# Kernel optimization log

Hardware: AMD Instinct MI355X
Metric: run time of the kernel (lower is better)

The kernel has to match this reference:

```python
import jax, jax.numpy as jnp
import numpy as np

B, N, L, E, U, G, R, D, C = 64, 50000, 8, 100000, 20000, 20000, 64, 16, 2


def setup_inputs() -> dict:
    rng = np.random.default_rng(0)
    key = jax.random.key(0)
    ks = jax.random.split(key, 10)
    # index structures (duplicate-free where the torch code assumes uniqueness)
    gene_map = jnp.asarray(rng.choice(N, G, replace=False).astype(np.int32))
    dst_unique = jnp.stack([jnp.asarray(rng.choice(N, U, replace=False).astype(np.int32)) for _ in range(L)])
    root_ids = jnp.asarray(rng.choice(N, R, replace=False).astype(np.int32))
    src = jax.random.randint(ks[0], (L, E), 0, N, dtype=jnp.int32)
    dst_pos = jax.random.randint(ks[1], (L, E), 0, U, dtype=jnp.int32)
    # data and parameters
    X_gene_batch = jax.random.normal(ks[2], (B, G), jnp.float32)
    w_in = jax.random.normal(ks[3], (D,), jnp.float32) * 0.5   # Linear(1, d) weight
    b_in = jax.random.normal(ks[4], (D,), jnp.float32) * 0.1
    W = jax.random.normal(ks[5], (L, D, D), jnp.float32) * (1.0 / np.sqrt(D))  # xavier-ish
    bias = jnp.zeros((N, D), jnp.float32)
    W_head = jax.random.normal(ks[6], (C, R * D), jnp.float32) * (1.0 / np.sqrt(R * D))
    b_head = jnp.zeros((C,), jnp.float32)
    return {
        "X_gene_batch": X_gene_batch, "w_in": w_in, "b_in": b_in, "W": W,
        "bias": bias, "W_head": W_head, "b_head": b_head,
        "gene_map": gene_map, "src": src, "dst_pos": dst_pos,
        "dst_unique": dst_unique, "root_ids": root_ids,
    }


def reference(X_gene_batch, w_in, b_in, W, bias, W_head, b_head,
              gene_map, src, dst_pos, dst_unique, root_ids):
    Bn = X_gene_batch.shape[0]
    n_nodes, d = bias.shape
    n_layers = W.shape[0]
    u = dst_unique.shape[1]
    # _init_state_vector: h=0, scatter in_proj(X[...,None]) at gene_map
    gene_emb = X_gene_batch[..., None] * w_in + b_in          # [B, G, d]
    h = jnp.zeros((Bn, n_nodes, d), X_gene_batch.dtype)
    h = h.at[:, gene_map].set(gene_emb)
    for li in range(n_layers):
        h_src = h[:, src[li]]                                  # gather [B, E, d]
        msg = jnp.einsum('bed,df->bef', h_src, W[li])          # small dxd matmul
        agg = jnp.zeros((Bn, u, d), h.dtype).at[:, dst_pos[li]].add(msg)  # scatter-add
        h_dst = jnp.tanh(agg + bias[dst_unique[li]][None])     # bias lookup + tanh (dropout=0)
        h = h.at[:, dst_unique[li]].set(h_dst)                 # write back
    feat = h[:, root_ids].reshape(Bn, -1)                      # roots_concat readout
    return feat @ W_head.T + b_head                            # [B, C]
```

## Files before the change

### kernel.cpp

```cpp
#include <hip/hip_runtime.h>
#include <hip/hip_fp16.h>
#include <cmath>

constexpr int B_ = 64, N_ = 50000, L_ = 8, E_ = 100000, U_ = 20000, G_ = 20000, R_ = 64, D_ = 16, C_ = 2;
constexpr int EPL_ = E_ + 3 * U_ + 4096;
constexpr int EPLG_ = EPL_ / 4 + 64;
constexpr int GPW = 8;
constexpr int GCAP = EPL_ / 4;
constexpr int SW = (GCAP + GPW - 1) / GPW;

constexpr int BC = 64;
constexpr int F = BC * 2;

constexpr int HBC = 32;
constexpr int FH = HBC * 2;
constexpr int DST0 = 1 + G_;
constexpr int AROWS = DST0 + L_ * U_;

__device__ __forceinline__ float tanh_fast(float x) {
  float e = __expf(2.0f * x);
  return 1.0f - 2.0f * __builtin_amdgcn_rcpf(e + 1.0f);
}


__global__ __launch_bounds__(256) void hist_kernel(
    const int* __restrict__ dst_pos, int* __restrict__ cnt,
    int* __restrict__ rank) {
  int e = blockIdx.x * 256 + threadIdx.x;
  int li = blockIdx.y;
  if (e >= E_) return;
  rank[li * E_ + e] = atomicAdd(&cnt[li * U_ + dst_pos[li * E_ + e]], 1);
}

__global__ __launch_bounds__(1024) void scan_kernel(
    const int* __restrict__ cnt, int* __restrict__ offs) {
  __shared__ int sums[1024];
  int li = blockIdx.x, t = threadIdx.x;
  int base = t * 20;
  int v[20];
  int s = 0;
#pragma unroll
  for (int i = 0; i < 20; ++i) {
    int idx = base + i;
    int c = (idx < U_) ? cnt[li * U_ + idx] : -1;
    int pc = (c < 0) ? 0 : ((c == 0) ? 4 : ((c + 3) & ~3));
    v[i] = s;
    s += pc;
  }
  sums[t] = s;
  __syncthreads();
  for (int off = 1; off < 1024; off <<= 1) {
    int o = (t >= off) ? sums[t - off] : 0;
    __syncthreads();
    sums[t] += o;
    __syncthreads();
  }
  int excl = sums[t] - s;
#pragma unroll
  for (int i = 0; i < 20; ++i) {
    int idx = base + i;
    if (idx < U_) offs[li * (U_ + 1) + idx] = excl + v[i];
  }
  if (t == 1023) offs[li * (U_ + 1) + U_] = sums[1023];
}

__global__ __launch_bounds__(256) void scatter_kernel(
    const int* __restrict__ dst_pos, const int* __restrict__ src,
    const int* __restrict__ offs, const int* __restrict__ rank,
    int* __restrict__ ssrc) {
  int e = blockIdx.x * 256 + threadIdx.x;
  int li = blockIdx.y;
  if (e >= E_) return;
  int u = dst_pos[li * E_ + e];
  int p = offs[li * (U_ + 1) + u] + rank[li * E_ + e];
  ssrc[(size_t)li * EPL_ + p] = src[li * E_ + e];
}

__global__ __launch_bounds__(256) void pad_fill_ug_k(
    const int* __restrict__ cnt, const int* __restrict__ offs,
    int* __restrict__ ssrc, int* __restrict__ ug) {
  int t = blockIdx.x * 256 + threadIdx.x;
  if (t < L_ * U_) {
    int li = t / U_, u = t % U_;
    int start = offs[li * (U_ + 1) + u];
    int end = start + cnt[li * U_ + u];
    int pend = offs[li * (U_ + 1) + u + 1];
    int* sp = ssrc + (size_t)li * EPL_;
    for (int p = end; p < pend; ++p) sp[p] = N_;
    int* ugp = ug + (size_t)li * EPLG_;
    for (int g = start >> 2; g < (pend >> 2); ++g) ugp[g] = u;
  } else {
    int t2 = t - L_ * U_;
    int li = t2 >> 8, j = t2 & 255;
    if (li < L_) {
      int* sp = ssrc + (size_t)li * EPL_;
      int ptot = offs[li * (U_ + 1) + U_];
      int pos = ptot + j;
      if (pos < EPL_) sp[pos] = N_;
      sp[EPL_ - 256 + j] = N_;
    }
  }
}


__global__ __launch_bounds__(256) void mark_k(
    const int* __restrict__ dst_unique, const int* __restrict__ gene_map,
    int* __restrict__ wmask, int* __restrict__ posarr, int* __restrict__ lw0) {
  int t = blockIdx.x * 256 + threadIdx.x;
  if (t < L_ * U_) {
    int li = t / U_, u = t % U_;
    int n = dst_unique[t];
    posarr[li * N_ + n] = u;
    atomicOr(&wmask[n], 1 << li);
  } else {
    int g = t - L_ * U_;
    if (g < G_) lw0[gene_map[g]] = 1 + g;
  }
}

__global__ __launch_bounds__(256) void remap_k(
    const int* __restrict__ offs, const int* __restrict__ wmask,
    const int* __restrict__ posarr, const int* __restrict__ lw0,
    int* __restrict__ ssrc) {
  int p = blockIdx.x * 256 + threadIdx.x;
  int li = blockIdx.y;
  if (p >= EPL_) return;
  int ptot = offs[li * (U_ + 1) + U_];
  if (p >= ptot + 256 && p < EPL_ - 256) return;
  int* sp = ssrc + (size_t)li * EPL_;
  int s = sp[p];
  int m = wmask[s] & ((1 << li) - 1);
  int phys;
  if (m) {
    int lj = 31 - __clz(m);
    phys = DST0 + lj * U_ + posarr[lj * N_ + s];
  } else {
    phys = lw0[s];
  }
  sp[p] = phys;
}

#define PHASE(VACC, VLD, IDLD, IDPF, NUCUR)          \
  {                                                  \
    loadRows(VLD, IDLD);                             \
    IDPF = *(const int4*)(sp + 4 * CLG(g + 4));      \
    int nuCur = NUCUR;                               \
    NUCUR = ugp[CLG(g + 3) + 1];                     \
    accum(VACC);                                     \
    if (nuCur != curU) {                             \
      flushu(curU);                                  \
      if (g + 1 >= gstop) return;                    \
      curU = nuCur;                                  \
    }                                                \
    ++g;                                             \
  }


__global__ __launch_bounds__(256) void gene_a(
    const float* __restrict__ X, const float* __restrict__ w_in,
    const float* __restrict__ b_in, float4* __restrict__ h4, int half) {
  int t = blockIdx.x * 256 + threadIdx.x;
  if (t >= G_ * HBC) return;
  int b = t % HBC;
  int g = t / HBC;
  float x = X[(half * HBC + b) * G_ + g];
  float4 out[2];
  __half2* oh = reinterpret_cast<__half2*>(out);
#pragma unroll
  for (int k = 0; k < 8; ++k) {
    float r0 = fmaf(x, w_in[2 * k], b_in[2 * k]);
    float r1 = fmaf(x, w_in[2 * k + 1], b_in[2 * k + 1]);
    oh[k] = __float22half2_rn(make_float2(r0, r1));
  }
  h4[(size_t)(1 + g) * FH + b * 2] = out[0];
  h4[(size_t)(1 + g) * FH + b * 2 + 1] = out[1];
}

__global__ __launch_bounds__(256, 2) void gfused_a(
    const float4* __restrict__ h4, const int* __restrict__ ug,
    const int* __restrict__ ssrc, const float* __restrict__ W,
    const float* __restrict__ bias, const int* __restrict__ dst_unique,
    float4* __restrict__ o4, int li) {
  __shared__ float Wlds[256];
  int tid = threadIdx.x;
  Wlds[tid] = W[li * 256 + tid];
  __syncthreads();
  int lane = tid & 63;
  int dh = lane & 1;
  int wv = __builtin_amdgcn_readfirstlane(blockIdx.x * 4 + (tid >> 6));
  const int* ugp = ug + (size_t)li * EPLG_;
  const int* sp = ssrc + (size_t)li * EPL_;
  const int* du = dst_unique + (size_t)li * U_;

  int g0 = wv * GPW, gend = g0 + GPW;
  int prevU = (g0 == 0) ? -2 : ugp[g0 - 1];
  int g = g0;
  while (g < gend && ugp[g] == prevU) ++g;
  if (g >= gend) return;
  int curU = ugp[g];
  if (curU < 0) return;
  int uend = ugp[gend - 1];
  int gstop;
  if (uend < 0) {
    gstop = g;
    while (ugp[gstop] >= 0) ++gstop;
  } else {
    gstop = gend;
    while (ugp[gstop] == uend) ++gstop;
  }

  __half2 acc[2][4];
  const __half2 z = __half2half2(__float2half(0.f));
#pragma unroll
  for (int j = 0; j < 2; ++j)
#pragma unroll
    for (int k = 0; k < 4; ++k) acc[j][k] = z;

  auto flushu = [&](int u) {
    int node = du[u];
    float biasv[8];
    {
      const float4* bp = (const float4*)(bias + (size_t)node * 16 + dh * 8);
      float4 q0 = bp[0], q1 = bp[1];
      biasv[0] = q0.x; biasv[1] = q0.y; biasv[2] = q0.z; biasv[3] = q0.w;
      biasv[4] = q1.x; biasv[5] = q1.y; biasv[6] = q1.z; biasv[7] = q1.w;
    }
    float a8[8];
#pragma unroll
    for (int k = 0; k < 4; ++k) {
      float2 f0 = __half22float2(acc[0][k]);
      float2 f1 = __half22float2(acc[1][k]);
      __half2 hv = __float22half2_rn(make_float2(f0.x + f1.x, f0.y + f1.y));
      float2 fa = __half22float2(hv);
      a8[2 * k] = fa.x; a8[2 * k + 1] = fa.y;
    }
    float pm[16];
#pragma unroll
    for (int j = 0; j < 16; ++j) pm[j] = 0.f;
#pragma unroll
    for (int dd = 0; dd < 8; ++dd) {
      float s = a8[dd];
      const float4* wr = (const float4*)&Wlds[(dh * 8 + dd) * 16];
      float4 w0 = wr[0], w1 = wr[1], w2 = wr[2], w3 = wr[3];
      pm[0] = fmaf(s, w0.x, pm[0]);  pm[1] = fmaf(s, w0.y, pm[1]);
      pm[2] = fmaf(s, w0.z, pm[2]);  pm[3] = fmaf(s, w0.w, pm[3]);
      pm[4] = fmaf(s, w1.x, pm[4]);  pm[5] = fmaf(s, w1.y, pm[5]);
      pm[6] = fmaf(s, w1.z, pm[6]);  pm[7] = fmaf(s, w1.w, pm[7]);
      pm[8] = fmaf(s, w2.x, pm[8]);  pm[9] = fmaf(s, w2.y, pm[9]);
      pm[10] = fmaf(s, w2.z, pm[10]); pm[11] = fmaf(s, w2.w, pm[11]);
      pm[12] = fmaf(s, w3.x, pm[12]); pm[13] = fmaf(s, w3.y, pm[13]);
      pm[14] = fmaf(s, w3.z, pm[14]); pm[15] = fmaf(s, w3.w, pm[15]);
    }
    float m8[8];
#pragma unroll
    for (int jj = 0; jj < 8; ++jj) {
      float s0 = pm[jj] + __shfl_xor(pm[jj], 1, 64);
      float s1 = pm[8 + jj] + __shfl_xor(pm[8 + jj], 1, 64);
      m8[jj] = dh ? s1 : s0;
    }
    float4 outv;
    __half2* ov = reinterpret_cast<__half2*>(&outv);
#pragma unroll
    for (int k = 0; k < 4; ++k) {
      ov[k] = __float22half2_rn(
          make_float2(tanh_fast(m8[2 * k] + biasv[2 * k]),
                      tanh_fast(m8[2 * k + 1] + biasv[2 * k + 1])));
    }
    o4[(size_t)(DST0 + li * U_ + u) * FH + lane] = outv;
#pragma unroll
    for (int j = 0; j < 2; ++j)
#pragma unroll
      for (int k = 0; k < 4; ++k) acc[j][k] = z;
  };

  auto loadRows = [&](float4 (&v)[4], int4 id) {
    v[0] = h4[(size_t)id.x * FH + lane];
    v[1] = h4[(size_t)id.y * FH + lane];
    v[2] = h4[(size_t)id.z * FH + lane];
    v[3] = h4[(size_t)id.w * FH + lane];
  };
  auto accum = [&](const float4 (&v)[4]) {
#pragma unroll
    for (int j = 0; j < 4; ++j) {
      const __half2* p = reinterpret_cast<const __half2*>(&v[j]);
#pragma unroll
      for (int k = 0; k < 4; ++k)
        acc[j & 1][k] = __hadd2(acc[j & 1][k], p[k]);
    }
  };
  auto CLG = [&](int q) { return (q < GCAP) ? q : GCAP - 1; };

  int4 id0 = *(const int4*)(sp + 4 * g);
  int4 id1 = *(const int4*)(sp + 4 * CLG(g + 1));
  int4 idP = *(const int4*)(sp + 4 * CLG(g + 2));
  int4 idQ = *(const int4*)(sp + 4 * CLG(g + 3));
  int4 idR;
  int nuA = ugp[g + 1];
  int nuB = ugp[CLG(g + 1) + 1];
  int nuC = ugp[CLG(g + 2) + 1];

  float4 va[4], vb[4], vc[4];
  loadRows(va, id0);
  loadRows(vb, id1);

  for (;;) {
    PHASE(va, vc, idP, idR, nuA)
    PHASE(vb, va, idQ, idP, nuB)
    PHASE(vc, vb, idR, idQ, nuC)
  }
}

__global__ __launch_bounds__(64) void head_a(
    const float4* __restrict__ h4, const float* __restrict__ W_head,
    const float* __restrict__ b_head, const int* __restrict__ root_ids,
    const int* __restrict__ wmask, const int* __restrict__ posarr,
    const int* __restrict__ lw0, int half, float* __restrict__ out) {
  int bl = blockIdx.x;
  int r = threadIdx.x;
  int node = root_ids[r];
  int m = wmask[node];
  int phys;
  if (m) {
    int lj = 31 - __clz(m);
    phys = DST0 + lj * U_ + posarr[lj * N_ + node];
  } else {
    phys = lw0[node];
  }
  float4 p0 = h4[(size_t)phys * FH + bl * 2];
  float4 p1 = h4[(size_t)phys * FH + bl * 2 + 1];
  float v[16];
  const __half2* ph0 = reinterpret_cast<const __half2*>(&p0);
  const __half2* ph1 = reinterpret_cast<const __half2*>(&p1);
#pragma unroll
  for (int k = 0; k < 4; ++k) {
    float2 f0 = __half22float2(ph0[k]);
    float2 f1 = __half22float2(ph1[k]);
    v[2 * k] = f0.x; v[2 * k + 1] = f0.y;
    v[8 + 2 * k] = f1.x; v[8 + 2 * k + 1] = f1.y;
  }
  float acc0 = 0.f, acc1 = 0.f;
#pragma unroll
  for (int d = 0; d < 16; ++d) {
    acc0 = fmaf(v[d], W_head[r * 16 + d], acc0);
    acc1 = fmaf(v[d], W_head[1024 + r * 16 + d], acc1);
  }
  for (int off = 32; off; off >>= 1) {
    acc0 += __shfl_down(acc0, off, 64);
    acc1 += __shfl_down(acc1, off, 64);
  }
  if (r == 0) {
    int gb = half * HBC + bl;
    out[gb * 2 + 0] = acc0 + b_head[0];
    out[gb * 2 + 1] = acc1 + b_head[1];
  }
}


__global__ __launch_bounds__(256) void gene_c(
    const float* __restrict__ X, const float* __restrict__ w_in,
    const float* __restrict__ b_in, const int* __restrict__ gene_map,
    float4* __restrict__ h4) {
  int t = blockIdx.x * 256 + threadIdx.x;
  if (t >= G_ * BC) return;
  int b = t % BC;
  int g = t / BC;
  float x = X[b * G_ + g];
  int node = gene_map[g];
  float4 out[2];
  __half2* oh = reinterpret_cast<__half2*>(out);
#pragma unroll
  for (int k = 0; k < 8; ++k) {
    float r0 = fmaf(x, w_in[2 * k], b_in[2 * k]);
    float r1 = fmaf(x, w_in[2 * k + 1], b_in[2 * k + 1]);
    oh[k] = __float22half2_rn(make_float2(r0, r1));
  }
  h4[(size_t)node * F + b * 2] = out[0];
  h4[(size_t)node * F + b * 2 + 1] = out[1];
}

__global__ __launch_bounds__(256, 2) void gather_c(
    const float4* __restrict__ h4, const int* __restrict__ ug,
    const int* __restrict__ ssrc, float4* __restrict__ agg4, int li) {
  int tid = threadIdx.x;
  int lane = tid & 63;
  int wv = __builtin_amdgcn_readfirstlane(blockIdx.x * 4 + (tid >> 6));
  const int* ugp = ug + (size_t)li * EPLG_;
  const int* sp = ssrc + (size_t)li * EPL_;

  int g0 = wv * GPW, gend = g0 + GPW;
  int prevU = (g0 == 0) ? -2 : ugp[g0 - 1];
  int g = g0;
  while (g < gend && ugp[g] == prevU) ++g;
  if (g >= gend) return;
  int curU = ugp[g];
  if (curU < 0) return;
  int uend = ugp[gend - 1];
  int gstop;
  if (uend < 0) {
    gstop = g;
    while (ugp[gstop] >= 0) ++gstop;
  } else {
    gstop = gend;
    while (ugp[gstop] == uend) ++gstop;
  }

  __half2 acc[2][2][4];
  const __half2 z = __half2half2(__float2half(0.f));
#pragma unroll
  for (int j = 0; j < 2; ++j)
#pragma unroll
    for (int r = 0; r < 2; ++r)
#pragma unroll
      for (int k = 0; k < 4; ++k) acc[j][r][k] = z;

  auto flushu = [&](int u) {
#pragma unroll
    for (int r = 0; r < 2; ++r) {
      float4 outv;
      __half2* ov = reinterpret_cast<__half2*>(&outv);
#pragma unroll
      for (int k = 0; k < 4; ++k) {
        float2 f0 = __half22float2(acc[0][r][k]);
        float2 f1 = __half22float2(acc[1][r][k]);
        ov[k] = __float22half2_rn(make_float2(f0.x + f1.x, f0.y + f1.y));
      }
      agg4[(size_t)u * F + lane + r * 64] = outv;
    }
#pragma unroll
    for (int j = 0; j < 2; ++j)
#pragma unroll
      for (int r = 0; r < 2; ++r)
#pragma unroll
        for (int k = 0; k < 4; ++k) acc[j][r][k] = z;
  };
  auto loadRows = [&](float4 (&v)[4][2], int4 id) {
    v[0][0] = h4[(size_t)id.x * F + lane]; v[0][1] = h4[(size_t)id.x * F + lane + 64];
    v[1][0] = h4[(size_t)id.y * F + lane]; v[1][1] = h4[(size_t)id.y * F + lane + 64];
    v[2][0] = h4[(size_t)id.z * F + lane]; v[2][1] = h4[(size_t)id.z * F + lane + 64];
    v[3][0] = h4[(size_t)id.w * F + lane]; v[3][1] = h4[(size_t)id.w * F + lane + 64];
  };
  auto accum = [&](const float4 (&v)[4][2]) {
#pragma unroll
    for (int j = 0; j < 4; ++j)
#pragma unroll
      for (int r = 0; r < 2; ++r) {
        const __half2* p = reinterpret_cast<const __half2*>(&v[j][r]);
#pragma unroll
        for (int k = 0; k < 4; ++k)
          acc[j & 1][r][k] = __hadd2(acc[j & 1][r][k], p[k]);
      }
  };
  auto CLG = [&](int q) { return (q < GCAP) ? q : GCAP - 1; };

  int4 id0 = *(const int4*)(sp + 4 * g);
  int4 id1 = *(const int4*)(sp + 4 * CLG(g + 1));
  int4 idP = *(const int4*)(sp + 4 * CLG(g + 2));
  int4 idQ = *(const int4*)(sp + 4 * CLG(g + 3));
  int4 idR;
  int nuA = ugp[g + 1];
  int nuB = ugp[CLG(g + 1) + 1];
  int nuC = ugp[CLG(g + 2) + 1];

  float4 va[4][2], vb[4][2], vc[4][2];
  loadRows(va, id0);
  loadRows(vb, id1);

  for (;;) {
    PHASE(va, vc, idP, idR, nuA)
    PHASE(vb, va, idQ, idP, nuB)
    PHASE(vc, vb, idR, idQ, nuC)
  }
}
#undef PHASE

__global__ __launch_bounds__(256) void dense_c(
    const float4* __restrict__ agg4, const float* __restrict__ W,
    const float* __restrict__ bias, const int* __restrict__ dst_unique,
    float4* __restrict__ h4, int li) {
  __shared__ float Wlds[256];
  int tid = threadIdx.x;
  Wlds[tid] = W[li * 256 + tid];
  __syncthreads();
  int u = __builtin_amdgcn_readfirstlane(blockIdx.x * 4 + (tid >> 6));
  int b = tid & 63;
  float4 c0 = agg4[(size_t)u * F + b * 2];
  float4 c1 = agg4[(size_t)u * F + b * 2 + 1];
  float a[16];
  {
    const __half2* p0 = reinterpret_cast<const __half2*>(&c0);
    const __half2* p1 = reinterpret_cast<const __half2*>(&c1);
#pragma unroll
    for (int k = 0; k < 4; ++k) {
      float2 f0 = __half22float2(p0[k]);
      float2 f1 = __half22float2(p1[k]);
      a[2 * k] = f0.x; a[2 * k + 1] = f0.y;
      a[8 + 2 * k] = f1.x; a[8 + 2 * k + 1] = f1.y;
    }
  }
  float m[16];
#pragma unroll
  for (int j = 0; j < 16; ++j) m[j] = 0.f;
#pragma unroll
  for (int d = 0; d < 16; ++d) {
    float s = a[d];
    const float4* wr = (const float4*)&Wlds[d * 16];
    float4 w0 = wr[0], w1 = wr[1], w2 = wr[2], w3 = wr[3];
    m[0] = fmaf(s, w0.x, m[0]);  m[1] = fmaf(s, w0.y, m[1]);
    m[2] = fmaf(s, w0.z, m[2]);  m[3] = fmaf(s, w0.w, m[3]);
    m[4] = fmaf(s, w1.x, m[4]);  m[5] = fmaf(s, w1.y, m[5]);
    m[6] = fmaf(s, w1.z, m[6]);  m[7] = fmaf(s, w1.w, m[7]);
    m[8] = fmaf(s, w2.x, m[8]);  m[9] = fmaf(s, w2.y, m[9]);
    m[10] = fmaf(s, w2.z, m[10]); m[11] = fmaf(s, w2.w, m[11]);
    m[12] = fmaf(s, w3.x, m[12]); m[13] = fmaf(s, w3.y, m[13]);
    m[14] = fmaf(s, w3.z, m[14]); m[15] = fmaf(s, w3.w, m[15]);
  }
  int node = dst_unique[li * U_ + u];
  const float4* bp = (const float4*)(bias + (size_t)node * 16);
  float4 b0 = bp[0], b1 = bp[1], b2 = bp[2], b3 = bp[3];
  float bb[16] = {b0.x, b0.y, b0.z, b0.w, b1.x, b1.y, b1.z, b1.w,
                  b2.x, b2.y, b2.z, b2.w, b3.x, b3.y, b3.z, b3.w};
  float4 o0, o1;
  __half2* ov0 = reinterpret_cast<__half2*>(&o0);
  __half2* ov1 = reinterpret_cast<__half2*>(&o1);
#pragma unroll
  for (int k = 0; k < 4; ++k) {
    ov0[k] = __float22half2_rn(make_float2(tanh_fast(m[2 * k] + bb[2 * k]),
                                           tanh_fast(m[2 * k + 1] + bb[2 * k + 1])));
    ov1[k] = __float22half2_rn(make_float2(tanh_fast(m[8 + 2 * k] + bb[8 + 2 * k]),
                                           tanh_fast(m[8 + 2 * k + 1] + bb[8 + 2 * k + 1])));
  }
  h4[(size_t)node * F + b * 2] = o0;
  h4[(size_t)node * F + b * 2 + 1] = o1;
}

__global__ __launch_bounds__(64) void head_c(
    const float4* __restrict__ h4, const float* __restrict__ W_head,
    const float* __restrict__ b_head, const int* __restrict__ root_ids,
    float* __restrict__ out) {
  int bl = blockIdx.x;
  int r = threadIdx.x;
  int node = root_ids[r];
  float4 p0 = h4[(size_t)node * F + bl * 2];
  float4 p1 = h4[(size_t)node * F + bl * 2 + 1];
  float v[16];
  const __half2* ph0 = reinterpret_cast<const __half2*>(&p0);
  const __half2* ph1 = reinterpret_cast<const __half2*>(&p1);
#pragma unroll
  for (int k = 0; k < 4; ++k) {
    float2 f0 = __half22float2(ph0[k]);
    float2 f1 = __half22float2(ph1[k]);
    v[2 * k] = f0.x; v[2 * k + 1] = f0.y;
    v[8 + 2 * k] = f1.x; v[8 + 2 * k + 1] = f1.y;
  }
  float acc0 = 0.f, acc1 = 0.f;
#pragma unroll
  for (int d = 0; d < 16; ++d) {
    acc0 = fmaf(v[d], W_head[r * 16 + d], acc0);
    acc1 = fmaf(v[d], W_head[1024 + r * 16 + d], acc1);
  }
  for (int off = 32; off; off >>= 1) {
    acc0 += __shfl_down(acc0, off, 64);
    acc1 += __shfl_down(acc1, off, 64);
  }
  if (r == 0) {
    out[bl * 2 + 0] = acc0 + b_head[0];
    out[bl * 2 + 1] = acc1 + b_head[1];
  }
}

__global__ void zero_out_k(float* out, int n) {
  int t = blockIdx.x * 256 + threadIdx.x;
  if (t < n) out[t] = 0.f;
}


static size_t csr_aux_bytes() {
  return (size_t)L_ * U_ * 4 +
         (size_t)L_ * (U_ + 1) * 4 +
         (size_t)L_ * E_ * 4 +
         (size_t)L_ * EPL_ * 4 +
         (size_t)L_ * EPLG_ * 4;
}
static size_t arena_bytes() {
  return (size_t)AROWS * FH * 16 + csr_aux_bytes() +
         (size_t)2 * (N_ + 1) * 4 +
         (size_t)L_ * N_ * 4;
}
static size_t classic_bytes() {
  return (size_t)(N_ + 1) * F * 16 + (size_t)U_ * F * 16 + csr_aux_bytes();
}

extern "C" void kernel_launch(void* const* d_in, const int* in_sizes, int n_in,
                              void* d_out, int out_size, void* d_ws, size_t ws_size,
                              hipStream_t stream) {
  const float* X = (const float*)d_in[0];
  const float* w_in = (const float*)d_in[1];
  const float* b_in = (const float*)d_in[2];
  const float* W = (const float*)d_in[3];
  const float* bias = (const float*)d_in[4];
  const float* W_head = (const float*)d_in[5];
  const float* b_head = (const float*)d_in[6];
  const int* gene_map = (const int*)d_in[7];
  const int* src = (const int*)d_in[8];
  const int* dst_pos = (const int*)d_in[9];
  const int* dst_unique = (const int*)d_in[10];
  const int* root_ids = (const int*)d_in[11];
  float* out = (float*)d_out;

  dim3 egrid((E_ + 255) / 256, L_);
  const int pf_grid = (L_ * U_ + L_ * 256 + 255) / 256;
  const int gather_grid = (SW + 3) / 4;

  if (ws_size >= arena_bytes()) {
    char* ws = (char*)d_ws;
    float4* arena = (float4*)ws;
    size_t off = (size_t)AROWS * FH * 16;
    int* cnt = (int*)(ws + off);    off += (size_t)L_ * U_ * 4;
    int* offs = (int*)(ws + off);   off += (size_t)L_ * (U_ + 1) * 4;
    int* rank = (int*)(ws + off);   off += (size_t)L_ * E_ * 4;
    int* ssrc = (int*)(ws + off);   off += (size_t)L_ * EPL_ * 4;
    int* ug = (int*)(ws + off);     off += (size_t)L_ * EPLG_ * 4;
    int* wmask = (int*)(ws + off);  off += (size_t)(N_ + 1) * 4;
    int* lw0 = (int*)(ws + off);    off += (size_t)(N_ + 1) * 4;
    int* posarr = (int*)(ws + off);

    hipMemsetAsync(cnt, 0, (size_t)L_ * U_ * 4, stream);
    hipMemsetAsync(ug, 0xFF, (size_t)L_ * EPLG_ * 4, stream);
    hipMemsetAsync(wmask, 0, (size_t)2 * (N_ + 1) * 4, stream);
    hipMemsetAsync(arena, 0, (size_t)FH * 16, stream);

    hist_kernel<<<egrid, 256, 0, stream>>>(dst_pos, cnt, rank);
    scan_kernel<<<L_, 1024, 0, stream>>>(cnt, offs);
    scatter_kernel<<<egrid, 256, 0, stream>>>(dst_pos, src, offs, rank, ssrc);
    pad_fill_ug_k<<<pf_grid, 256, 0, stream>>>(cnt, offs, ssrc, ug);
    mark_k<<<(L_ * U_ + G_ + 255) / 256, 256, 0, stream>>>(dst_unique, gene_map,
                                                           wmask, posarr, lw0);
    dim3 rgrid((EPL_ + 255) / 256, L_);
    remap_k<<<rgrid, 256, 0, stream>>>(offs, wmask, posarr, lw0, ssrc);

    for (int half = 0; half < 2; ++half) {
      gene_a<<<(G_ * HBC + 255) / 256, 256, 0, stream>>>(X, w_in, b_in, arena,
                                                         half);
      for (int li = 0; li < L_; ++li) {
        gfused_a<<<gather_grid, 256, 0, stream>>>(arena, ug, ssrc, W, bias,
                                                  dst_unique, arena, li);
      }
      head_a<<<HBC, 64, 0, stream>>>(arena, W_head, b_head, root_ids, wmask,
                                     posarr, lw0, half, out);
    }
  } else if (ws_size >= classic_bytes()) {
    const size_t h_bytes = (size_t)(N_ + 1) * F * 16;
    const size_t agg_bytes = (size_t)U_ * F * 16;
    char* ws = (char*)d_ws;
    float4* h4 = (float4*)ws;
    float4* agg4 = (float4*)(ws + h_bytes);
    size_t off = h_bytes + agg_bytes;
    int* cnt = (int*)(ws + off);  off += (size_t)L_ * U_ * 4;
    int* offs = (int*)(ws + off); off += (size_t)L_ * (U_ + 1) * 4;
    int* rank = (int*)(ws + off); off += (size_t)L_ * E_ * 4;
    int* ssrc = (int*)(ws + off); off += (size_t)L_ * EPL_ * 4;
    int* ug = (int*)(ws + off);

    hipMemsetAsync(cnt, 0, (size_t)L_ * U_ * 4, stream);
    hipMemsetAsync(ug, 0xFF, (size_t)L_ * EPLG_ * 4, stream);
    hipMemsetAsync(h4, 0, h_bytes, stream);
    hist_kernel<<<egrid, 256, 0, stream>>>(dst_pos, cnt, rank);
    scan_kernel<<<L_, 1024, 0, stream>>>(cnt, offs);
    scatter_kernel<<<egrid, 256, 0, stream>>>(dst_pos, src, offs, rank, ssrc);
    pad_fill_ug_k<<<pf_grid, 256, 0, stream>>>(cnt, offs, ssrc, ug);
    gene_c<<<(G_ * BC + 255) / 256, 256, 0, stream>>>(X, w_in, b_in, gene_map, h4);
    const int dense_grid = U_ * BC / 256;
    for (int li = 0; li < L_; ++li) {
      gather_c<<<gather_grid, 256, 0, stream>>>(h4, ug, ssrc, agg4, li);
      dense_c<<<dense_grid, 256, 0, stream>>>(agg4, W, bias, dst_unique, h4, li);
    }
    head_c<<<BC, 64, 0, stream>>>(h4, W_head, b_head, root_ids, out);
  } else {
    zero_out_k<<<(out_size + 255) / 256, 256, 0, stream>>>(out, out_size);
  }
}
```

Before: 550.7 us.

## Fuse CSR preprocessing kernels and coalesce gene embedding input reads

Merges histogram and node-marking into one launch. Replaces the stored per-edge rank with an atomic cursor on a copy of the offsets, so remapping to arena rows happens inside the scatter, and folds the ug fill and zero-row setup into the pad kernel, removing several memsets and the separate mark and remap passes. gene_a now stages X through shared memory so global reads are coalesced along the G dimension. The cost is atomic position assignment, which makes edge order within each destination segment nondeterministic, and that can change float summation order.

Result: slower. 568.8 us (+3.3%).

```diff
diff --git a/kernel.cpp b/kernel.cpp
--- a/kernel.cpp
+++ b/kernel.cpp
@@ -8,6 +8,7 @@
 constexpr int GPW = 8;
 constexpr int GCAP = EPL_ / 4;
 constexpr int SW = (GCAP + GPW - 1) / GPW;
+constexpr int HISTB = (E_ + 255) / 256;
 
 constexpr int BC = 64;
 constexpr int F = BC * 2;
@@ -23,17 +24,32 @@
 }
 
 
-__global__ __launch_bounds__(256) void hist_kernel(
+__global__ __launch_bounds__(256) void hist_mark_k(
     const int* __restrict__ dst_pos, int* __restrict__ cnt,
-    int* __restrict__ rank) {
-  int e = blockIdx.x * 256 + threadIdx.x;
+    const int* __restrict__ dst_unique, const int* __restrict__ gene_map,
+    int* __restrict__ wmask, int* __restrict__ posarr, int* __restrict__ lw0) {
   int li = blockIdx.y;
-  if (e >= E_) return;
-  rank[li * E_ + e] = atomicAdd(&cnt[li * U_ + dst_pos[li * E_ + e]], 1);
+  int bx = blockIdx.x;
+  if (bx < HISTB) {
+    int e = bx * 256 + threadIdx.x;
+    if (e < E_) atomicAdd(&cnt[li * U_ + dst_pos[li * E_ + e]], 1);
+  } else if (li == 0) {
+    int t = (bx - HISTB) * 256 + threadIdx.x;
+    if (t < L_ * U_) {
+      int lj = t / U_, u = t % U_;
+      int n = dst_unique[t];
+      posarr[lj * N_ + n] = u;
+      atomicOr(&wmask[n], 1 << lj);
+    } else {
+      int g = t - L_ * U_;
+      if (g < G_) lw0[gene_map[g]] = 1 + g;
+    }
+  }
 }
 
 __global__ __launch_bounds__(1024) void scan_kernel(
-    const int* __restrict__ cnt, int* __restrict__ offs) {
+    const int* __restrict__ cnt, int* __restrict__ offs,
+    int* __restrict__ woffs) {
   __shared__ int sums[1024];
   int li = blockIdx.x, t = threadIdx.x;
   int base = t * 20;
@@ -59,76 +75,26 @@
 #pragma unroll
   for (int i = 0; i < 20; ++i) {
     int idx = base + i;
-    if (idx < U_) offs[li * (U_ + 1) + idx] = excl + v[i];
+    if (idx < U_) {
+      int sv = excl + v[i];
+      offs[li * (U_ + 1) + idx] = sv;
+      woffs[li * (U_ + 1) + idx] = sv;
+    }
   }
   if (t == 1023) offs[li * (U_ + 1) + U_] = sums[1023];
 }
 
-__global__ __launch_bounds__(256) void scatter_kernel(
+__global__ __launch_bounds__(256) void scatter_arena_k(
     const int* __restrict__ dst_pos, const int* __restrict__ src,
-    const int* __restrict__ offs, const int* __restrict__ rank,
+    int* __restrict__ woffs, const int* __restrict__ wmask,
+    const int* __restrict__ posarr, const int* __restrict__ lw0,
     int* __restrict__ ssrc) {
   int e = blockIdx.x * 256 + threadIdx.x;
   int li = blockIdx.y;
   if (e >= E_) return;
   int u = dst_pos[li * E_ + e];
-  int p = offs[li * (U_ + 1) + u] + rank[li * E_ + e];
-  ssrc[(size_t)li * EPL_ + p] = src[li * E_ + e];
-}
-
-__global__ __launch_bounds__(256) void pad_fill_ug_k(
-    const int* __restrict__ cnt, const int* __restrict__ offs,
-    int* __restrict__ ssrc, int* __restrict__ ug) {
-  int t = blockIdx.x * 256 + threadIdx.x;
-  if (t < L_ * U_) {
-    int li = t / U_, u = t % U_;
-    int start = offs[li * (U_ + 1) + u];
-    int end = start + cnt[li * U_ + u];
-    int pend = offs[li * (U_ + 1) + u + 1];
-    int* sp = ssrc + (size_t)li * EPL_;
-    for (int p = end; p < pend; ++p) sp[p] = N_;
-    int* ugp = ug + (size_t)li * EPLG_;
-    for (int g = start >> 2; g < (pend >> 2); ++g) ugp[g] = u;
-  } else {
-    int t2 = t - L_ * U_;
-    int li = t2 >> 8, j = t2 & 255;
-    if (li < L_) {
-      int* sp = ssrc + (size_t)li * EPL_;
-      int ptot = offs[li * (U_ + 1) + U_];
-      int pos = ptot + j;
-      if (pos < EPL_) sp[pos] = N_;
-      sp[EPL_ - 256 + j] = N_;
-    }
-  }
-}
-
-
-__global__ __launch_bounds__(256) void mark_k(
-    const int* __restrict__ dst_unique, const int* __restrict__ gene_map,
-    int* __restrict__ wmask, int* __restrict__ posarr, int* __restrict__ lw0) {
-  int t = blockIdx.x * 256 + threadIdx.x;
-  if (t < L_ * U_) {
-    int li = t / U_, u = t % U_;
-    int n = dst_unique[t];
-    posarr[li * N_ + n] = u;
-    atomicOr(&wmask[n], 1 << li);
-  } else {
-    int g = t - L_ * U_;
-    if (g < G_) lw0[gene_map[g]] = 1 + g;
-  }
-}
-
-__global__ __launch_bounds__(256) void remap_k(
-    const int* __restrict__ offs, const int* __restrict__ wmask,
-    const int* __restrict__ posarr, const int* __restrict__ lw0,
-    int* __restrict__ ssrc) {
-  int p = blockIdx.x * 256 + threadIdx.x;
-  int li = blockIdx.y;
-  if (p >= EPL_) return;
-  int ptot = offs[li * (U_ + 1) + U_];
-  if (p >= ptot + 256 && p < EPL_ - 256) return;
-  int* sp = ssrc + (size_t)li * EPL_;
-  int s = sp[p];
+  int p = atomicAdd(&woffs[li * (U_ + 1) + u], 1);
+  int s = src[li * E_ + e];
   int m = wmask[s] & ((1 << li) - 1);
   int phys;
   if (m) {
@@ -137,7 +103,50 @@
   } else {
     phys = lw0[s];
   }
-  sp[p] = phys;
+  ssrc[(size_t)li * EPL_ + p] = phys;
+}
+
+__global__ __launch_bounds__(256) void scatter_classic_k(
+    const int* __restrict__ dst_pos, const int* __restrict__ src,
+    int* __restrict__ woffs, int* __restrict__ ssrc) {
+  int e = blockIdx.x * 256 + threadIdx.x;
+  int li = blockIdx.y;
+  if (e >= E_) return;
+  int u = dst_pos[li * E_ + e];
+  int p = atomicAdd(&woffs[li * (U_ + 1) + u], 1);
+  ssrc[(size_t)li * EPL_ + p] = src[li * E_ + e];
+}
+
+__global__ __launch_bounds__(256) void pad_fill_ug_k(
+    const int* __restrict__ woffs, const int* __restrict__ offs,
+    int* __restrict__ ssrc, int* __restrict__ ug, int sentinel,
+    float4* __restrict__ zrow) {
+  int t = blockIdx.x * 256 + threadIdx.x;
+  if (t < L_ * U_) {
+    int li = t / U_, u = t % U_;
+    int start = offs[li * (U_ + 1) + u];
+    int end = woffs[li * (U_ + 1) + u];
+    int pend = offs[li * (U_ + 1) + u + 1];
+    int* sp = ssrc + (size_t)li * EPL_;
+    for (int p = end; p < pend; ++p) sp[p] = sentinel;
+    int* ugp = ug + (size_t)li * EPLG_;
+    for (int g = start >> 2; g < (pend >> 2); ++g) ugp[g] = u;
+  } else {
+    int t2 = t - L_ * U_;
+    int li = t2 >> 10, j = t2 & 1023;
+    if (li < L_) {
+      int* sp = ssrc + (size_t)li * EPL_;
+      int ptot = offs[li * (U_ + 1) + U_];
+      if (j < 256) {
+        int pos = ptot + j;
+        if (pos < EPL_) sp[pos] = sentinel;
+        sp[EPL_ - 256 + j] = sentinel;
+      }
+      int* ugp = ug + (size_t)li * EPLG_;
+      for (int gq = (ptot >> 2) + j; gq < EPLG_; gq += 1024) ugp[gq] = -1;
+      if (li == 0 && j < FH && zrow) zrow[j] = make_float4(0.f, 0.f, 0.f, 0.f);
+    }
+  }
 }
 
 #define PHASE(VACC, VLD, IDLD, IDPF, NUCUR)          \
@@ -159,11 +168,18 @@
 __global__ __launch_bounds__(256) void gene_a(
     const float* __restrict__ X, const float* __restrict__ w_in,
     const float* __restrict__ b_in, float4* __restrict__ h4, int half) {
-  int t = blockIdx.x * 256 + threadIdx.x;
-  if (t >= G_ * HBC) return;
-  int b = t % HBC;
-  int g = t / HBC;
-  float x = X[(half * HBC + b) * G_ + g];
+  __shared__ float xs[8][33];
+  int tid = threadIdx.x;
+  int g0 = blockIdx.x * 8;
+  {
+    int b = tid >> 3, gi = tid & 7;
+    xs[gi][b] = X[(size_t)(half * HBC + b) * G_ + g0 + gi];
+  }
+  __syncthreads();
+  int b = tid & 31;
+  int gi = tid >> 5;
+  float x = xs[gi][b];
+  int g = g0 + gi;
   float4 out[2];
   __half2* oh = reinterpret_cast<__half2*>(out);
 #pragma unroll
@@ -574,20 +590,19 @@
 }
 
 
-static size_t csr_aux_bytes() {
-  return (size_t)L_ * U_ * 4 +
-         (size_t)L_ * (U_ + 1) * 4 +
-         (size_t)L_ * E_ * 4 +
+static size_t arena_bytes() {
+  return (size_t)AROWS * FH * 16 +
+         (size_t)L_ * U_ * 4 +
+         (size_t)2 * (N_ + 1) * 4 +
+         (size_t)L_ * (U_ + 1) * 4 * 2 +
          (size_t)L_ * EPL_ * 4 +
-         (size_t)L_ * EPLG_ * 4;
-}
-static size_t arena_bytes() {
-  return (size_t)AROWS * FH * 16 + csr_aux_bytes() +
-         (size_t)2 * (N_ + 1) * 4 +
+         (size_t)L_ * EPLG_ * 4 +
          (size_t)L_ * N_ * 4;
 }
 static size_t classic_bytes() {
-  return (size_t)(N_ + 1) * F * 16 + (size_t)U_ * F * 16 + csr_aux_bytes();
+  return (size_t)(N_ + 1) * F * 16 + (size_t)U_ * F * 16 +
+         (size_t)L_ * U_ * 4 + (size_t)L_ * (U_ + 1) * 4 * 2 +
+         (size_t)L_ * EPL_ * 4 + (size_t)L_ * EPLG_ * 4;
 }
 
 extern "C" void kernel_launch(void* const* d_in, const int* in_sizes, int n_in,
@@ -607,8 +622,8 @@
   const int* root_ids = (const int*)d_in[11];
   float* out = (float*)d_out;
 
-  dim3 egrid((E_ + 255) / 256, L_);
-  const int pf_grid = (L_ * U_ + L_ * 256 + 255) / 256;
+  dim3 egrid(HISTB, L_);
+  const int pf_grid = (L_ * U_ + L_ * 1024 + 255) / 256;
   const int gather_grid = (SW + 3) / 4;
 
   if (ws_size >= arena_bytes()) {
@@ -616,31 +631,26 @@
     float4* arena = (float4*)ws;
     size_t off = (size_t)AROWS * FH * 16;
     int* cnt = (int*)(ws + off);    off += (size_t)L_ * U_ * 4;
+    int* wmask = (int*)(ws + off);  off += (size_t)(N_ + 1) * 4;
+    int* lw0 = (int*)(ws + off);    off += (size_t)(N_ + 1) * 4;
     int* offs = (int*)(ws + off);   off += (size_t)L_ * (U_ + 1) * 4;
-    int* rank = (int*)(ws + off);   off += (size_t)L_ * E_ * 4;
+    int* woffs = (int*)(ws + off);  off += (size_t)L_ * (U_ + 1) * 4;
     int* ssrc = (int*)(ws + off);   off += (size_t)L_ * EPL_ * 4;
     int* ug = (int*)(ws + off);     off += (size_t)L_ * EPLG_ * 4;
-    int* wmask = (int*)(ws + off);  off += (size_t)(N_ + 1) * 4;
-    int* lw0 = (int*)(ws + off);    off += (size_t)(N_ + 1) * 4;
     int* posarr = (int*)(ws + off);
 
-    hipMemsetAsync(cnt, 0, (size_t)L_ * U_ * 4, stream);
-    hipMemsetAsync(ug, 0xFF, (size_t)L_ * EPLG_ * 4, stream);
-    hipMemsetAsync(wmask, 0, (size_t)2 * (N_ + 1) * 4, stream);
-    hipMemsetAsync(arena, 0, (size_t)FH * 16, stream);
-
-    hist_kernel<<<egrid, 256, 0, stream>>>(dst_pos, cnt, rank);
-    scan_kernel<<<L_, 1024, 0, stream>>>(cnt, offs);
-    scatter_kernel<<<egrid, 256, 0, stream>>>(dst_pos, src, offs, rank, ssrc);
-    pad_fill_ug_k<<<pf_grid, 256, 0, stream>>>(cnt, offs, ssrc, ug);
-    mark_k<<<(L_ * U_ + G_ + 255) / 256, 256, 0, stream>>>(dst_unique, gene_map,
-                                                           wmask, posarr, lw0);
-    dim3 rgrid((EPL_ + 255) / 256, L_);
-    remap_k<<<rgrid, 256, 0, stream>>>(offs, wmask, posarr, lw0, ssrc);
+    hipMemsetAsync(cnt, 0, (size_t)L_ * U_ * 4 + (size_t)2 * (N_ + 1) * 4,
+                   stream);
+    dim3 hmgrid(HISTB + (L_ * U_ + G_ + 255) / 256, L_);
+    hist_mark_k<<<hmgrid, 256, 0, stream>>>(dst_pos, cnt, dst_unique, gene_map,
+                                            wmask, posarr, lw0);
+    scan_kernel<<<L_, 1024, 0, stream>>>(cnt, offs, woffs);
+    scatter_arena_k<<<egrid, 256, 0, stream>>>(dst_pos, src, woffs, wmask,
+                                               posarr, lw0, ssrc);
+    pad_fill_ug_k<<<pf_grid, 256, 0, stream>>>(woffs, offs, ssrc, ug, 0, arena);
 
     for (int half = 0; half < 2; ++half) {
-      gene_a<<<(G_ * HBC + 255) / 256, 256, 0, stream>>>(X, w_in, b_in, arena,
-                                                         half);
+      gene_a<<<G_ / 8, 256, 0, stream>>>(X, w_in, b_in, arena, half);
       for (int li = 0; li < L_; ++li) {
         gfused_a<<<gather_grid, 256, 0, stream>>>(arena, ug, ssrc, W, bias,
                                                   dst_unique, arena, li);
@@ -655,19 +665,20 @@
     float4* h4 = (float4*)ws;
     float4* agg4 = (float4*)(ws + h_bytes);
     size_t off = h_bytes + agg_bytes;
-    int* cnt = (int*)(ws + off);  off += (size_t)L_ * U_ * 4;
-    int* offs = (int*)(ws + off); off += (size_t)L_ * (U_ + 1) * 4;
-    int* rank = (int*)(ws + off); off += (size_t)L_ * E_ * 4;
-    int* ssrc = (int*)(ws + off); off += (size_t)L_ * EPL_ * 4;
+    int* cnt = (int*)(ws + off);   off += (size_t)L_ * U_ * 4;
+    int* offs = (int*)(ws + off);  off += (size_t)L_ * (U_ + 1) * 4;
+    int* woffs = (int*)(ws + off); off += (size_t)L_ * (U_ + 1) * 4;
+    int* ssrc = (int*)(ws + off);  off += (size_t)L_ * EPL_ * 4;
     int* ug = (int*)(ws + off);
 
     hipMemsetAsync(cnt, 0, (size_t)L_ * U_ * 4, stream);
-    hipMemsetAsync(ug, 0xFF, (size_t)L_ * EPLG_ * 4, stream);
     hipMemsetAsync(h4, 0, h_bytes, stream);
-    hist_kernel<<<egrid, 256, 0, stream>>>(dst_pos, cnt, rank);
-    scan_kernel<<<L_, 1024, 0, stream>>>(cnt, offs);
-    scatter_kernel<<<egrid, 256, 0, stream>>>(dst_pos, src, offs, rank, ssrc);
-    pad_fill_ug_k<<<pf_grid, 256, 0, stream>>>(cnt, offs, ssrc, ug);
+    hist_mark_k<<<egrid, 256, 0, stream>>>(dst_pos, cnt, nullptr, nullptr,
+                                           nullptr, nullptr, nullptr);
+    scan_kernel<<<L_, 1024, 0, stream>>>(cnt, offs, woffs);
+    scatter_classic_k<<<egrid, 256, 0, stream>>>(dst_pos, src, woffs, ssrc);
+    pad_fill_ug_k<<<pf_grid, 256, 0, stream>>>(woffs, offs, ssrc, ug, N_,
+                                               nullptr);
     gene_c<<<(G_ * BC + 255) / 256, 256, 0, stream>>>(X, w_in, b_in, gene_map, h4);
     const int dense_grid = U_ * BC / 256;
     for (int li = 0; li < L_; ++li) {
```
